# Performance work log

Measured on AMD Instinct MI355X. Metric: run time of the kernel, lower is better.

The kernel has to match this reference:

```python
import jax, jax.numpy as jnp
import numpy as np

N_NODES = 50000
NEG_SLOPE = 0.2  # PyG GATConv default leaky_relu slope


def gat_layer(x, edge_index, W, a_src, a_dst, bias, heads, out_dim, concat):
    """PyG-style GATConv with self-loops.
    x: [N, F_in]; edge_index: [2, E]; W: [F_in, heads*out_dim];
    a_src, a_dst: [heads, out_dim]; bias: [heads*out_dim] or [out_dim].
    """
    N = x.shape[0]
    # add self loops (PyG default add_self_loops=True)
    ar = jnp.arange(N, dtype=edge_index.dtype)
    ei = jnp.concatenate([edge_index, jnp.stack([ar, ar])], axis=1)
    src, dst = ei[0], ei[1]

    h = (x @ W).reshape(N, heads, out_dim)            # [N, H, F]
    alpha_src = jnp.einsum('nhf,hf->nh', h, a_src)    # [N, H]
    alpha_dst = jnp.einsum('nhf,hf->nh', h, a_dst)

    e = alpha_src[src] + alpha_dst[dst]               # [E, H]
    e = jax.nn.leaky_relu(e, NEG_SLOPE)

    # segment softmax over incoming edges of each dst node
    m = jax.ops.segment_max(e, dst, num_segments=N)   # [N, H]
    ex = jnp.exp(e - m[dst])
    denom = jax.ops.segment_sum(ex, dst, num_segments=N)
    alpha = ex / denom[dst]                           # [E, H]

    msg = alpha[:, :, None] * h[src]                  # [E, H, F]
    out = jax.ops.segment_sum(msg, dst, num_segments=N)  # [N, H, F]

    if concat:
        out = out.reshape(N, heads * out_dim)
    else:
        out = out.mean(axis=1)
    return out + bias


def setup_inputs() -> dict:
    key = jax.random.key(0)
    ks = jax.random.split(key, 10)
    node_dim, hidden = 128, 64
    x = jax.random.normal(ks[0], (N_NODES, node_dim), dtype=jnp.float32)
    edge_index = jax.random.randint(ks[1], (2, 600000), 0, N_NODES, dtype=jnp.int64)
    s1 = 1.0 / np.sqrt(node_dim)
    s2 = 1.0 / np.sqrt(2 * hidden)
    return {
        'x': x,
        'edge_index': edge_index,
        'W1': jax.random.normal(ks[2], (node_dim, 2 * hidden), dtype=jnp.float32) * s1,
        'a_src1': jax.random.normal(ks[3], (2, hidden), dtype=jnp.float32) * s1,
        'a_dst1': jax.random.normal(ks[4], (2, hidden), dtype=jnp.float32) * s1,
        'b1': jnp.zeros((2 * hidden,), dtype=jnp.float32),
        'W2': jax.random.normal(ks[5], (2 * hidden, hidden), dtype=jnp.float32) * s2,
        'a_src2': jax.random.normal(ks[6], (1, hidden), dtype=jnp.float32) * s2,
        'a_dst2': jax.random.normal(ks[7], (1, hidden), dtype=jnp.float32) * s2,
        'b2': jnp.zeros((hidden,), dtype=jnp.float32),
    }


def reference(x, edge_index, W1, a_src1, a_dst1, b1, W2, a_src2, a_dst2, b2):
    h = gat_layer(x, edge_index, W1, a_src1, a_dst1, b1, heads=2, out_dim=64, concat=True)
    h = jax.nn.elu(h)
    out = gat_layer(h, edge_index, W2, a_src2, a_dst2, b2, heads=1, out_dim=64, concat=False)
    return out
```

## Files before the change

### kernel.cpp

```cpp
#include <hip/hip_runtime.h>
#include <hip/hip_bf16.h>


#define LRELU_SLOPE 0.2f

typedef __bf16 v8bf __attribute__((ext_vector_type(8)));
typedef float f32x4 __attribute__((ext_vector_type(4)));


__device__ __forceinline__ unsigned short bf16r(float x) {
    unsigned u = __float_as_uint(x);
    return (unsigned short)((u + 0x7fff + ((u >> 16) & 1)) >> 16);
}
__device__ __forceinline__ unsigned pbf(float a, float b) {
    return (unsigned)bf16r(a) | ((unsigned)bf16r(b) << 16);
}
__device__ __forceinline__ float bflo(unsigned u) { return __uint_as_float(u << 16); }
__device__ __forceinline__ float bfhi(unsigned u) { return __uint_as_float(u & 0xffff0000u); }

__device__ __forceinline__ v8bf ldfrag(const char* base, int row, int kb) {
    uint4 u = *(const uint4*)(base + row * 256 + (kb ^ ((row & 7) << 4)));
    return __builtin_bit_cast(v8bf, u);
}
__device__ __forceinline__ v8bf ldwt(const unsigned short* wt, int n, int kb) {
    uint4 u = *(const uint4*)((const char*)wt + n * 256 + kb);
    return __builtin_bit_cast(v8bf, u);
}


__global__ void prep_kernel(const float* __restrict__ W1, const float* __restrict__ W2,
                            unsigned short* __restrict__ wt1,
                            unsigned short* __restrict__ wt2,
                            int* __restrict__ deg, int N) {
    int b = blockIdx.x, tid = threadIdx.x;
    if (b < 3) {
        int id = b * 256 + tid;
        int n = id >> 2, kq = id & 3;
        if (n < 128) {
            #pragma unroll 8
            for (int j = 0; j < 32; j++) {
                int k = kq * 32 + j;
                wt1[n * 128 + k] = bf16r(W1[k * 128 + n]);
            }
        } else if (n < 192) {
            int n2 = n - 128;
            #pragma unroll 8
            for (int j = 0; j < 32; j++) {
                int k = kq * 32 + j;
                wt2[n2 * 128 + k] = bf16r(W2[k * 64 + n2]);
            }
        }
    } else {
        int i = (b - 3) * 256 + tid;
        if (i < N) deg[i] = 0;
    }
}


__global__ void degree_kernel(const int* __restrict__ ei, int E,
                              int* __restrict__ deg) {
    int t4 = (blockIdx.x * 256 + threadIdx.x) * 4;
    if (t4 + 3 < E) {
        int4 d4 = *(const int4*)(ei + E + t4);
        atomicAdd(&deg[d4.x], 1);
        atomicAdd(&deg[d4.y], 1);
        atomicAdd(&deg[d4.z], 1);
        atomicAdd(&deg[d4.w], 1);
    } else {
        for (int j = 0; j < 4; j++) {
            int e = t4 + j;
            if (e < E) atomicAdd(&deg[ei[E + e]], 1);
        }
    }
}


__global__ void scan1_kernel(const int* __restrict__ deg, int* __restrict__ row_ptr,
                             int* __restrict__ bsum, int n) {
    __shared__ int sm[16];
    int tid = threadIdx.x;
    int i = blockIdx.x * 1024 + tid;
    int v = (i < n) ? deg[i] + 1 : 0;
    int lane = tid & 63, wid = tid >> 6;
    int s = v;
    #pragma unroll
    for (int o = 1; o < 64; o <<= 1) { int t = __shfl_up(s, o); if (lane >= o) s += t; }
    if (lane == 63) sm[wid] = s;
    __syncthreads();
    if (tid < 16) {
        int ws = sm[tid];
        #pragma unroll
        for (int o = 1; o < 16; o <<= 1) { int t = __shfl_up(ws, o); if (tid >= o) ws += t; }
        sm[tid] = ws;
    }
    __syncthreads();
    int excl = (wid ? sm[wid - 1] : 0) + s - v;
    if (i < n) row_ptr[i] = excl;
    if (tid == 1023) bsum[blockIdx.x] = excl + v;
}


__global__ void scan23_kernel(int* __restrict__ row_ptr, int* __restrict__ cursor,
                              unsigned short* __restrict__ srcs,
                              const int* __restrict__ bsum,
                              const int* __restrict__ deg, int n, int nb) {
    __shared__ int boff_sm;
    int tid = threadIdx.x;
    if (tid < 64) {
        int v = (tid < nb) ? bsum[tid] : 0;
        int s = v;
        #pragma unroll
        for (int o = 1; o < 64; o <<= 1) { int t = __shfl_up(s, o); if (tid >= o) s += t; }
        if (tid == blockIdx.x) boff_sm = s - v;
    }
    __syncthreads();
    int boff = boff_sm;
    int i = blockIdx.x * 1024 + tid;
    if (i >= n) return;
    int val = row_ptr[i] + boff;
    row_ptr[i] = val;
    cursor[i]  = val + 1;
    srcs[val]  = (unsigned short)i;
    if (i == n - 1) row_ptr[n] = val + deg[i] + 1;
}


__global__ __launch_bounds__(256) void sg_kernel(const float* __restrict__ X,
        const unsigned short* __restrict__ wt, const float* __restrict__ asw,
        const float* __restrict__ adw, unsigned short* __restrict__ hb,
        float* __restrict__ as_out, float* __restrict__ ad_out, int M, int GS,
        const int* __restrict__ ei, int E, int* __restrict__ cursor,
        unsigned short* __restrict__ srcs) {
    __shared__ uint4 xs4[1024];
    __shared__ float aps[4][64], apd[4][64];
    int t = threadIdx.x;

    if (blockIdx.x < GS) {
        int t4 = (blockIdx.x * 256 + t) * 4;
        if (t4 + 3 < E) {
            int4 s4 = *(const int4*)(ei + t4);
            int4 d4 = *(const int4*)(ei + E + t4);
            int p0 = atomicAdd(&cursor[d4.x], 1);
            int p1 = atomicAdd(&cursor[d4.y], 1);
            int p2 = atomicAdd(&cursor[d4.z], 1);
            int p3 = atomicAdd(&cursor[d4.w], 1);
            srcs[p0] = (unsigned short)s4.x;
            srcs[p1] = (unsigned short)s4.y;
            srcs[p2] = (unsigned short)s4.z;
            srcs[p3] = (unsigned short)s4.w;
        } else {
            for (int j = 0; j < 4; j++) {
                int e = t4 + j;
                if (e < E) {
                    int pos = atomicAdd(&cursor[ei[E + e]], 1);
                    srcs[pos] = (unsigned short)ei[e];
                }
            }
        }
        return;
    }

    char* xs = (char*)xs4;
    int row0 = (blockIdx.x - GS) * 64;
    int lane = t & 63, w = t >> 6;

    {
        int kq = t & 31;
        for (int m = t >> 5; m < 64; m += 8) {
            int gr = row0 + m;
            float4 v = make_float4(0.f, 0.f, 0.f, 0.f);
            if (gr < M) v = *(const float4*)(X + (size_t)gr * 128 + kq * 4);
            *(uint2*)(xs + m * 256 + ((kq * 8) ^ ((m & 7) << 4))) =
                make_uint2(pbf(v.x, v.y), pbf(v.z, v.w));
        }
    }
    __syncthreads();

    int l15 = lane & 15, lhi = lane >> 4;
    f32x4 acc[4][2];
    #pragma unroll
    for (int rt = 0; rt < 4; rt++) { acc[rt][0] = (f32x4)(0.f); acc[rt][1] = (f32x4)(0.f); }

    #pragma unroll
    for (int ks = 0; ks < 4; ks++) {
        int kb = ks * 64 + lhi * 16;
        v8bf b0 = ldwt(wt, w * 32 + l15, kb);
        v8bf b1 = ldwt(wt, w * 32 + 16 + l15, kb);
        #pragma unroll
        for (int rt = 0; rt < 4; rt++) {
            v8bf a = ldfrag(xs, rt * 16 + l15, kb);
            acc[rt][0] = __builtin_amdgcn_mfma_f32_16x16x32_bf16(a, b0, acc[rt][0], 0, 0, 0);
            acc[rt][1] = __builtin_amdgcn_mfma_f32_16x16x32_bf16(a, b1, acc[rt][1], 0, 0, 0);
        }
    }

    float asv0 = asw[w * 32 + l15],      adv0 = adw[w * 32 + l15];
    float asv1 = asw[w * 32 + 16 + l15], adv1 = adw[w * 32 + 16 + l15];
    #pragma unroll
    for (int rt = 0; rt < 4; rt++) {
        #pragma unroll
        for (int r = 0; r < 4; r++) {
            int m = rt * 16 + lhi * 4 + r;
            int gr = row0 + m;
            float v0 = acc[rt][0][r], v1 = acc[rt][1][r];
            if (gr < M) {
                hb[(size_t)gr * 128 + w * 32 + l15]      = bf16r(v0);
                hb[(size_t)gr * 128 + w * 32 + 16 + l15] = bf16r(v1);
            }
            float ps = v0 * asv0 + v1 * asv1;
            float pd = v0 * adv0 + v1 * adv1;
            #pragma unroll
            for (int o = 1; o < 16; o <<= 1) { ps += __shfl_xor(ps, o); pd += __shfl_xor(pd, o); }
            if (l15 == 0) { aps[w][m] = ps; apd[w][m] = pd; }
        }
    }
    __syncthreads();
    if (t < 128) {
        int m = t & 63, hd = t >> 6;
        int gr = row0 + m;
        if (gr < M) {
            as_out[gr * 2 + hd] = aps[hd * 2][m] + aps[hd * 2 + 1][m];
            ad_out[gr * 2 + hd] = apd[hd * 2][m] + apd[hd * 2 + 1][m];
        }
    }
}


__global__ __launch_bounds__(256) void gemm2_kernel(const unsigned short* __restrict__ X,
        const unsigned short* __restrict__ wt, const float* __restrict__ asw,
        const float* __restrict__ adw, unsigned short* __restrict__ hb2,
        float* __restrict__ as_out, float* __restrict__ ad_out, int M) {
    __shared__ uint4 xs4[1024];
    __shared__ float aps[4][64], apd[4][64];
    char* xs = (char*)xs4;
    int t = threadIdx.x;
    int row0 = blockIdx.x * 64;
    int lane = t & 63, w = t >> 6;

    {
        int slot = t & 15;
        for (int m = t >> 4; m < 64; m += 16) {
            int gr = row0 + m;
            uint4 v = make_uint4(0, 0, 0, 0);
            if (gr < M) v = *(const uint4*)(X + (size_t)gr * 128 + slot * 8);
            *(uint4*)(xs + m * 256 + ((slot * 16) ^ ((m & 7) << 4))) = v;
        }
    }
    __syncthreads();

    int l15 = lane & 15, lhi = lane >> 4;
    f32x4 acc[4];
    #pragma unroll
    for (int rt = 0; rt < 4; rt++) acc[rt] = (f32x4)(0.f);

    #pragma unroll
    for (int ks = 0; ks < 4; ks++) {
        int kb = ks * 64 + lhi * 16;
        v8bf b0 = ldwt(wt, w * 16 + l15, kb);
        #pragma unroll
        for (int rt = 0; rt < 4; rt++) {
            v8bf a = ldfrag(xs, rt * 16 + l15, kb);
            acc[rt] = __builtin_amdgcn_mfma_f32_16x16x32_bf16(a, b0, acc[rt], 0, 0, 0);
        }
    }

    float asv = asw[w * 16 + l15], adv = adw[w * 16 + l15];
    #pragma unroll
    for (int rt = 0; rt < 4; rt++) {
        #pragma unroll
        for (int r = 0; r < 4; r++) {
            int m = rt * 16 + lhi * 4 + r;
            int gr = row0 + m;
            float v0 = acc[rt][r];
            if (gr < M) hb2[(size_t)gr * 64 + w * 16 + l15] = bf16r(v0);
            float ps = v0 * asv;
            float pd = v0 * adv;
            #pragma unroll
            for (int o = 1; o < 16; o <<= 1) { ps += __shfl_xor(ps, o); pd += __shfl_xor(pd, o); }
            if (l15 == 0) { aps[w][m] = ps; apd[w][m] = pd; }
        }
    }
    __syncthreads();
    if (t < 64) {
        int gr = row0 + t;
        if (gr < M) {
            as_out[gr] = aps[0][t] + aps[1][t] + aps[2][t] + aps[3][t];
            ad_out[gr] = apd[0][t] + apd[1][t] + apd[2][t] + apd[3][t];
        }
    }
}


__global__ __launch_bounds__(256) void agg1_kernel(const uint4* __restrict__ hb,
        const float2* __restrict__ asrc, const float2* __restrict__ adst,
        const int* __restrict__ row_ptr, const unsigned short* __restrict__ srcs,
        const float* __restrict__ bias, unsigned short* __restrict__ helu_b, int N) {
    int tid = threadIdx.x, wid = tid >> 6, lane = tid & 63;
    int n = blockIdx.x * 4 + wid;
    if (n >= N) return;
    int chunk = lane & 15;
    int slot  = lane >> 4;
    int start = row_ptr[n];
    int deg   = row_ptr[n + 1] - start;
    float2 ad = adst[n];

    float acc[8];
    #pragma unroll
    for (int k = 0; k < 8; k++) acc[k] = 0.f;
    float dsum0 = 0.f, dsum1 = 0.f;

    for (int base = 0; base < deg; base += 64) {
        int cnt = min(64, deg - base);
        int s = 0; float w0 = 0.f, w1 = 0.f;
        if (lane < cnt) {
            s = srcs[start + base + lane];
            float2 av = asrc[s];
            float e0 = av.x + ad.x; e0 = (e0 >= 0.f) ? e0 : LRELU_SLOPE * e0;
            float e1 = av.y + ad.y; e1 = (e1 >= 0.f) ? e1 : LRELU_SLOPE * e1;
            w0 = __expf(e0); w1 = __expf(e1);
        }
        dsum0 += w0; dsum1 += w1;

        for (int j0 = 0; j0 < cnt; j0 += 8) {
            int ea = j0 + slot, eb = j0 + 4 + slot;
            int sa = __shfl(s, ea), sb = __shfl(s, eb);
            float wa0 = __shfl(w0, ea), wa1 = __shfl(w1, ea);
            float wb0 = __shfl(w0, eb), wb1 = __shfl(w1, eb);
            float wa = (chunk >= 8) ? wa1 : wa0;
            float wb = (chunk >= 8) ? wb1 : wb0;
            uint4 ua = make_uint4(0, 0, 0, 0), ub = make_uint4(0, 0, 0, 0);
            if (ea < cnt) ua = hb[(size_t)sa * 16 + chunk];
            if (eb < cnt) ub = hb[(size_t)sb * 16 + chunk];
            acc[0] += wa * bflo(ua.x) + wb * bflo(ub.x);
            acc[1] += wa * bfhi(ua.x) + wb * bfhi(ub.x);
            acc[2] += wa * bflo(ua.y) + wb * bflo(ub.y);
            acc[3] += wa * bfhi(ua.y) + wb * bfhi(ub.y);
            acc[4] += wa * bflo(ua.z) + wb * bflo(ub.z);
            acc[5] += wa * bfhi(ua.z) + wb * bfhi(ub.z);
            acc[6] += wa * bflo(ua.w) + wb * bflo(ub.w);
            acc[7] += wa * bfhi(ua.w) + wb * bfhi(ub.w);
        }
    }

    #pragma unroll
    for (int k = 0; k < 8; k++) {
        acc[k] += __shfl_xor(acc[k], 16);
        acc[k] += __shfl_xor(acc[k], 32);
    }
    #pragma unroll
    for (int o = 1; o < 64; o <<= 1) {
        dsum0 += __shfl_xor(dsum0, o);
        dsum1 += __shfl_xor(dsum1, o);
    }
    if (slot == 0) {
        float inv = 1.f / ((chunk >= 8) ? dsum1 : dsum0);
        int f = chunk * 8;
        float q[8];
        #pragma unroll
        for (int k = 0; k < 8; k++) {
            q[k] = acc[k] * inv + bias[f + k];
            q[k] = (q[k] > 0.f) ? q[k] : __expf(q[k]) - 1.f;
        }
        *(uint4*)&helu_b[(size_t)n * 128 + f] = make_uint4(
            pbf(q[0], q[1]), pbf(q[2], q[3]), pbf(q[4], q[5]), pbf(q[6], q[7]));
    }
}


__global__ __launch_bounds__(256) void agg2_kernel(const uint4* __restrict__ hb2,
        const float* __restrict__ asrc, const float* __restrict__ adst,
        const int* __restrict__ row_ptr, const unsigned short* __restrict__ srcs,
        const float* __restrict__ bias, float* __restrict__ out, int N) {
    int tid = threadIdx.x, wid = tid >> 6, lane = tid & 63;
    int n = blockIdx.x * 4 + wid;
    if (n >= N) return;
    int chunk = lane & 7;
    int slot  = lane >> 3;
    int start = row_ptr[n];
    int deg   = row_ptr[n + 1] - start;
    float ad = adst[n];

    float acc[8];
    #pragma unroll
    for (int k = 0; k < 8; k++) acc[k] = 0.f;
    float dsum = 0.f;

    for (int base = 0; base < deg; base += 64) {
        int cnt = min(64, deg - base);
        int s = 0; float w = 0.f;
        if (lane < cnt) {
            s = srcs[start + base + lane];
            float e = asrc[s] + ad;
            e = (e >= 0.f) ? e : LRELU_SLOPE * e;
            w = __expf(e);
        }
        dsum += w;

        for (int j0 = 0; j0 < cnt; j0 += 16) {
            int ea = j0 + slot, eb = j0 + 8 + slot;
            int sa = __shfl(s, ea), sb = __shfl(s, eb);
            float wa = __shfl(w, ea), wb = __shfl(w, eb);
            uint4 ua = make_uint4(0, 0, 0, 0), ub = make_uint4(0, 0, 0, 0);
            if (ea < cnt) ua = hb2[(size_t)sa * 8 + chunk];
            if (eb < cnt) ub = hb2[(size_t)sb * 8 + chunk];
            acc[0] += wa * bflo(ua.x) + wb * bflo(ub.x);
            acc[1] += wa * bfhi(ua.x) + wb * bfhi(ub.x);
            acc[2] += wa * bflo(ua.y) + wb * bflo(ub.y);
            acc[3] += wa * bfhi(ua.y) + wb * bfhi(ub.y);
            acc[4] += wa * bflo(ua.z) + wb * bflo(ub.z);
            acc[5] += wa * bfhi(ua.z) + wb * bfhi(ub.z);
            acc[6] += wa * bflo(ua.w) + wb * bflo(ub.w);
            acc[7] += wa * bfhi(ua.w) + wb * bfhi(ub.w);
        }
    }

    #pragma unroll
    for (int k = 0; k < 8; k++) {
        acc[k] += __shfl_xor(acc[k], 8);
        acc[k] += __shfl_xor(acc[k], 16);
        acc[k] += __shfl_xor(acc[k], 32);
    }
    #pragma unroll
    for (int o = 1; o < 64; o <<= 1) dsum += __shfl_xor(dsum, o);
    if (slot == 0) {
        float inv = 1.f / dsum;
        int f = chunk * 8;
        float q[8];
        #pragma unroll
        for (int k = 0; k < 8; k++) q[k] = acc[k] * inv + bias[f + k];
        *(float4*)&out[(size_t)n * 64 + f]     = make_float4(q[0], q[1], q[2], q[3]);
        *(float4*)&out[(size_t)n * 64 + f + 4] = make_float4(q[4], q[5], q[6], q[7]);
    }
}


extern "C" void kernel_launch(void* const* d_in, const int* in_sizes, int n_in,
                              void* d_out, int out_size, void* d_ws, size_t ws_size,
                              hipStream_t stream) {
    const float* x    = (const float*)d_in[0];
    const int*   ei   = (const int*)d_in[1];
    const float* W1   = (const float*)d_in[2];
    const float* as1w = (const float*)d_in[3];
    const float* ad1w = (const float*)d_in[4];
    const float* b1   = (const float*)d_in[5];
    const float* W2   = (const float*)d_in[6];
    const float* as2w = (const float*)d_in[7];
    const float* ad2w = (const float*)d_in[8];
    const float* b2   = (const float*)d_in[9];
    float* out = (float*)d_out;

    const int N  = in_sizes[0] / 128;
    const int E  = in_sizes[1] / 2;
    const int ET = E + N;

    char* base = (char*)d_ws;
    size_t off = 0;
    auto alloc = [&](size_t bytes) -> void* {
        void* p = base + off;
        off += (bytes + 255) & ~(size_t)255;
        return p;
    };
    unsigned short* hb1  = (unsigned short*)alloc((size_t)N * 128 * 2);
    unsigned short* hbel = (unsigned short*)alloc((size_t)N * 128 * 2);
    unsigned short* hb2  = (unsigned short*)alloc((size_t)N * 64 * 2);
    float* as1     = (float*)alloc((size_t)N * 2 * 4);
    float* ad1     = (float*)alloc((size_t)N * 2 * 4);
    float* as2     = (float*)alloc((size_t)N * 4);
    float* ad2     = (float*)alloc((size_t)N * 4);
    int*   deg     = (int*)alloc((size_t)N * 4);
    int*   row_ptr = (int*)alloc((size_t)(N + 1) * 4);
    int*   cursor  = (int*)alloc((size_t)(N + 1) * 4);
    unsigned short* srcs = (unsigned short*)alloc((size_t)ET * 2);
    int*   bsum    = (int*)alloc(64 * 4);
    unsigned short* wt1 = (unsigned short*)alloc(128 * 128 * 2);
    unsigned short* wt2 = (unsigned short*)alloc(64 * 128 * 2);

    const int G1 = (N + 63) / 64;
    const int GS = (E / 4 + 255) / 256;
    const int SCAN_B = (N + 1023) / 1024;

    prep_kernel<<<3 + (N + 255) / 256, 256, 0, stream>>>(W1, W2, wt1, wt2, deg, N);
    degree_kernel<<<GS, 256, 0, stream>>>(ei, E, deg);
    scan1_kernel<<<SCAN_B, 1024, 0, stream>>>(deg, row_ptr, bsum, N);
    scan23_kernel<<<SCAN_B, 1024, 0, stream>>>(row_ptr, cursor, srcs, bsum, deg,
                                               N, SCAN_B);
    sg_kernel<<<GS + G1, 256, 0, stream>>>(x, wt1, as1w, ad1w, hb1, as1, ad1,
                                           N, GS, ei, E, cursor, srcs);
    agg1_kernel<<<(N + 3) / 4, 256, 0, stream>>>((const uint4*)hb1,
                                                 (const float2*)as1, (const float2*)ad1,
                                                 row_ptr, srcs, b1, hbel, N);
    gemm2_kernel<<<(N + 63) / 64, 256, 0, stream>>>(hbel, wt2, as2w, ad2w,
                                                    hb2, as2, ad2, N);
    agg2_kernel<<<(N + 3) / 4, 256, 0, stream>>>((const uint4*)hb2, as2, ad2,
                                                 row_ptr, srcs, b2, out, N);
}
```

Measured before the change: 154.9 us.

## Fuse degree counting into layer-1 GEMM kernel and split out CSR scatter

The edge-degree atomics now run in extra blocks of the layer-1 GEMM kernel, placed after the GEMM blocks, instead of sharing a kernel with the CSR scatter. The scatter becomes its own kernel after the scans and handles 8 edges per thread using nontemporal stores. The aim is to overlap the GEMM with degree counting and to shorten the serial preprocessing chain, at the cost of a separate, lightweight scatter launch.

```diff
diff --git a/kernel.cpp b/kernel.cpp
--- a/kernel.cpp
+++ b/kernel.cpp
@@ -57,111 +57,35 @@
 }
 
 
-__global__ void degree_kernel(const int* __restrict__ ei, int E,
-                              int* __restrict__ deg) {
-    int t4 = (blockIdx.x * 256 + threadIdx.x) * 4;
-    if (t4 + 3 < E) {
-        int4 d4 = *(const int4*)(ei + E + t4);
-        atomicAdd(&deg[d4.x], 1);
-        atomicAdd(&deg[d4.y], 1);
-        atomicAdd(&deg[d4.z], 1);
-        atomicAdd(&deg[d4.w], 1);
-    } else {
-        for (int j = 0; j < 4; j++) {
-            int e = t4 + j;
-            if (e < E) atomicAdd(&deg[ei[E + e]], 1);
-        }
-    }
-}
-
-
-__global__ void scan1_kernel(const int* __restrict__ deg, int* __restrict__ row_ptr,
-                             int* __restrict__ bsum, int n) {
-    __shared__ int sm[16];
-    int tid = threadIdx.x;
-    int i = blockIdx.x * 1024 + tid;
-    int v = (i < n) ? deg[i] + 1 : 0;
-    int lane = tid & 63, wid = tid >> 6;
-    int s = v;
-    #pragma unroll
-    for (int o = 1; o < 64; o <<= 1) { int t = __shfl_up(s, o); if (lane >= o) s += t; }
-    if (lane == 63) sm[wid] = s;
-    __syncthreads();
-    if (tid < 16) {
-        int ws = sm[tid];
-        #pragma unroll
-        for (int o = 1; o < 16; o <<= 1) { int t = __shfl_up(ws, o); if (tid >= o) ws += t; }
-        sm[tid] = ws;
-    }
-    __syncthreads();
-    int excl = (wid ? sm[wid - 1] : 0) + s - v;
-    if (i < n) row_ptr[i] = excl;
-    if (tid == 1023) bsum[blockIdx.x] = excl + v;
-}
-
-
-__global__ void scan23_kernel(int* __restrict__ row_ptr, int* __restrict__ cursor,
-                              unsigned short* __restrict__ srcs,
-                              const int* __restrict__ bsum,
-                              const int* __restrict__ deg, int n, int nb) {
-    __shared__ int boff_sm;
-    int tid = threadIdx.x;
-    if (tid < 64) {
-        int v = (tid < nb) ? bsum[tid] : 0;
-        int s = v;
-        #pragma unroll
-        for (int o = 1; o < 64; o <<= 1) { int t = __shfl_up(s, o); if (tid >= o) s += t; }
-        if (tid == blockIdx.x) boff_sm = s - v;
-    }
-    __syncthreads();
-    int boff = boff_sm;
-    int i = blockIdx.x * 1024 + tid;
-    if (i >= n) return;
-    int val = row_ptr[i] + boff;
-    row_ptr[i] = val;
-    cursor[i]  = val + 1;
-    srcs[val]  = (unsigned short)i;
-    if (i == n - 1) row_ptr[n] = val + deg[i] + 1;
-}
-
-
-__global__ __launch_bounds__(256) void sg_kernel(const float* __restrict__ X,
+__global__ __launch_bounds__(256) void gd_kernel(const float* __restrict__ X,
         const unsigned short* __restrict__ wt, const float* __restrict__ asw,
         const float* __restrict__ adw, unsigned short* __restrict__ hb,
-        float* __restrict__ as_out, float* __restrict__ ad_out, int M, int GS,
-        const int* __restrict__ ei, int E, int* __restrict__ cursor,
-        unsigned short* __restrict__ srcs) {
+        float* __restrict__ as_out, float* __restrict__ ad_out, int M, int G1,
+        const int* __restrict__ ei, int E, int* __restrict__ deg) {
     __shared__ uint4 xs4[1024];
     __shared__ float aps[4][64], apd[4][64];
     int t = threadIdx.x;
 
-    if (blockIdx.x < GS) {
-        int t4 = (blockIdx.x * 256 + t) * 4;
-        if (t4 + 3 < E) {
-            int4 s4 = *(const int4*)(ei + t4);
-            int4 d4 = *(const int4*)(ei + E + t4);
-            int p0 = atomicAdd(&cursor[d4.x], 1);
-            int p1 = atomicAdd(&cursor[d4.y], 1);
-            int p2 = atomicAdd(&cursor[d4.z], 1);
-            int p3 = atomicAdd(&cursor[d4.w], 1);
-            srcs[p0] = (unsigned short)s4.x;
-            srcs[p1] = (unsigned short)s4.y;
-            srcs[p2] = (unsigned short)s4.z;
-            srcs[p3] = (unsigned short)s4.w;
+    if (blockIdx.x >= G1) {
+        int t8 = ((blockIdx.x - G1) * 256 + t) * 8;
+        if (t8 + 7 < E) {
+            int4 a = *(const int4*)(ei + E + t8);
+            int4 b = *(const int4*)(ei + E + t8 + 4);
+            atomicAdd(&deg[a.x], 1); atomicAdd(&deg[a.y], 1);
+            atomicAdd(&deg[a.z], 1); atomicAdd(&deg[a.w], 1);
+            atomicAdd(&deg[b.x], 1); atomicAdd(&deg[b.y], 1);
+            atomicAdd(&deg[b.z], 1); atomicAdd(&deg[b.w], 1);
         } else {
-            for (int j = 0; j < 4; j++) {
-                int e = t4 + j;
-                if (e < E) {
-                    int pos = atomicAdd(&cursor[ei[E + e]], 1);
-                    srcs[pos] = (unsigned short)ei[e];
-                }
+            for (int j = 0; j < 8; j++) {
+                int e = t8 + j;
+                if (e < E) atomicAdd(&deg[ei[E + e]], 1);
             }
         }
         return;
     }
 
     char* xs = (char*)xs4;
-    int row0 = (blockIdx.x - GS) * 64;
+    int row0 = blockIdx.x * 64;
     int lane = t & 63, w = t >> 6;
 
     {
@@ -221,6 +145,93 @@
         if (gr < M) {
             as_out[gr * 2 + hd] = aps[hd * 2][m] + aps[hd * 2 + 1][m];
             ad_out[gr * 2 + hd] = apd[hd * 2][m] + apd[hd * 2 + 1][m];
+        }
+    }
+}
+
+
+__global__ void scan1_kernel(const int* __restrict__ deg, int* __restrict__ row_ptr,
+                             int* __restrict__ bsum, int n) {
+    __shared__ int sm[16];
+    int tid = threadIdx.x;
+    int i = blockIdx.x * 1024 + tid;
+    int v = (i < n) ? deg[i] + 1 : 0;
+    int lane = tid & 63, wid = tid >> 6;
+    int s = v;
+    #pragma unroll
+    for (int o = 1; o < 64; o <<= 1) { int t = __shfl_up(s, o); if (lane >= o) s += t; }
+    if (lane == 63) sm[wid] = s;
+    __syncthreads();
+    if (tid < 16) {
+        int ws = sm[tid];
+        #pragma unroll
+        for (int o = 1; o < 16; o <<= 1) { int t = __shfl_up(ws, o); if (tid >= o) ws += t; }
+        sm[tid] = ws;
+    }
+    __syncthreads();
+    int excl = (wid ? sm[wid - 1] : 0) + s - v;
+    if (i < n) row_ptr[i] = excl;
+    if (tid == 1023) bsum[blockIdx.x] = excl + v;
+}
+
+
+__global__ void scan23_kernel(int* __restrict__ row_ptr, int* __restrict__ cursor,
+                              unsigned short* __restrict__ srcs,
+                              const int* __restrict__ bsum,
+                              const int* __restrict__ deg, int n, int nb) {
+    __shared__ int boff_sm;
+    int tid = threadIdx.x;
+    if (tid < 64) {
+        int v = (tid < nb) ? bsum[tid] : 0;
+        int s = v;
+        #pragma unroll
+        for (int o = 1; o < 64; o <<= 1) { int t = __shfl_up(s, o); if (tid >= o) s += t; }
+        if (tid == blockIdx.x) boff_sm = s - v;
+    }
+    __syncthreads();
+    int boff = boff_sm;
+    int i = blockIdx.x * 1024 + tid;
+    if (i >= n) return;
+    int val = row_ptr[i] + boff;
+    row_ptr[i] = val;
+    cursor[i]  = val + 1;
+    srcs[val]  = (unsigned short)i;
+    if (i == n - 1) row_ptr[n] = val + deg[i] + 1;
+}
+
+
+__global__ void scatter_kernel(const int* __restrict__ ei, int E,
+                               int* __restrict__ cursor,
+                               unsigned short* __restrict__ srcs) {
+    int t8 = (blockIdx.x * 256 + threadIdx.x) * 8;
+    if (t8 + 7 < E) {
+        int4 s0 = *(const int4*)(ei + t8);
+        int4 s1 = *(const int4*)(ei + t8 + 4);
+        int4 d0 = *(const int4*)(ei + E + t8);
+        int4 d1 = *(const int4*)(ei + E + t8 + 4);
+        int p0 = atomicAdd(&cursor[d0.x], 1);
+        int p1 = atomicAdd(&cursor[d0.y], 1);
+        int p2 = atomicAdd(&cursor[d0.z], 1);
+        int p3 = atomicAdd(&cursor[d0.w], 1);
+        int p4 = atomicAdd(&cursor[d1.x], 1);
+        int p5 = atomicAdd(&cursor[d1.y], 1);
+        int p6 = atomicAdd(&cursor[d1.z], 1);
+        int p7 = atomicAdd(&cursor[d1.w], 1);
+        __builtin_nontemporal_store((unsigned short)s0.x, &srcs[p0]);
+        __builtin_nontemporal_store((unsigned short)s0.y, &srcs[p1]);
+        __builtin_nontemporal_store((unsigned short)s0.z, &srcs[p2]);
+        __builtin_nontemporal_store((unsigned short)s0.w, &srcs[p3]);
+        __builtin_nontemporal_store((unsigned short)s1.x, &srcs[p4]);
+        __builtin_nontemporal_store((unsigned short)s1.y, &srcs[p5]);
+        __builtin_nontemporal_store((unsigned short)s1.z, &srcs[p6]);
+        __builtin_nontemporal_store((unsigned short)s1.w, &srcs[p7]);
+    } else {
+        for (int j = 0; j < 8; j++) {
+            int e = t8 + j;
+            if (e < E) {
+                int pos = atomicAdd(&cursor[ei[E + e]], 1);
+                srcs[pos] = (unsigned short)ei[e];
+            }
         }
     }
 }
@@ -476,16 +487,17 @@
     unsigned short* wt2 = (unsigned short*)alloc(64 * 128 * 2);
 
     const int G1 = (N + 63) / 64;
-    const int GS = (E / 4 + 255) / 256;
+    const int GD = (E / 8 + 255) / 256;
+    const int GS = GD;
     const int SCAN_B = (N + 1023) / 1024;
 
     prep_kernel<<<3 + (N + 255) / 256, 256, 0, stream>>>(W1, W2, wt1, wt2, deg, N);
-    degree_kernel<<<GS, 256, 0, stream>>>(ei, E, deg);
+    gd_kernel<<<G1 + GD, 256, 0, stream>>>(x, wt1, as1w, ad1w, hb1, as1, ad1,
+                                           N, G1, ei, E, deg);
     scan1_kernel<<<SCAN_B, 1024, 0, stream>>>(deg, row_ptr, bsum, N);
     scan23_kernel<<<SCAN_B, 1024, 0, stream>>>(row_ptr, cursor, srcs, bsum, deg,
                                                N, SCAN_B);
-    sg_kernel<<<GS + G1, 256, 0, stream>>>(x, wt1, as1w, ad1w, hb1, as1, ad1,
-                                           N, GS, ei, E, cursor, srcs);
+    scatter_kernel<<<GS, 256, 0, stream>>>(ei, E, cursor, srcs);
     agg1_kernel<<<(N + 3) / 4, 256, 0, stream>>>((const uint4*)hb1,
                                                  (const float2*)as1, (const float2*)ad1,
                                                  row_ptr, srcs, b1, hbel, N);
```

Result: slower. 159.0 us (+2.7%).
